# Kernel optimization log

Hardware: AMD Instinct MI355X
Metric: run time of the kernel (lower is better)

## Reference

```python
import jax, jax.numpy as jnp
import numpy as np

N_NODES = 100000


def gcn_conv(x, src, dst, W, b):
    # PyG GCNConv: add self-loops, symmetric deg^-1/2 normalization,
    # linear transform, scatter-add aggregation to target nodes, plus bias.
    n = x.shape[0]
    loops = jnp.arange(n, dtype=src.dtype)
    s = jnp.concatenate([src, loops])
    d = jnp.concatenate([dst, loops])
    deg = jax.ops.segment_sum(jnp.ones_like(s, dtype=x.dtype), d, num_segments=n)
    dinv = jnp.where(deg > 0, jax.lax.rsqrt(deg), 0.0)
    norm = dinv[s] * dinv[d]                       # [E+n]
    h = x @ W                                      # [n, out]
    msg = h[s] * norm[:, None]                     # gather + scale
    out = jax.ops.segment_sum(msg, d, num_segments=n)
    return out + b


def setup_inputs() -> dict:
    key = jax.random.key(0)
    k1, k2, k3, k4 = jax.random.split(key, 4)
    in_c, hid_c, out_c = 64, 64, 64
    n_edges = 1600000
    x = jax.random.normal(k1, (N_NODES, in_c), dtype=jnp.float32)
    edge_index = jax.random.randint(k2, (2, n_edges), 0, N_NODES, dtype=jnp.int64)
    W1 = jax.random.normal(k3, (in_c, hid_c), dtype=jnp.float32) * (1.0 / np.sqrt(in_c))
    b1 = jnp.zeros((hid_c,), dtype=jnp.float32)
    W2 = jax.random.normal(k4, (hid_c, out_c), dtype=jnp.float32) * (1.0 / np.sqrt(hid_c))
    b2 = jnp.zeros((out_c,), dtype=jnp.float32)
    return {"x": x, "edge_index": edge_index, "W1": W1, "b1": b1, "W2": W2, "b2": b2}


def reference(x, edge_index, W1, b1, W2, b2):
    src, dst = edge_index[0], edge_index[1]
    h = gcn_conv(x, src, dst, W1, b1)
    h = jax.nn.relu(h)
    out = gcn_conv(h, src, dst, W2, b2)
    return out
```

## Files before the change

kernel.cpp:

```cpp
#include <hip/hip_runtime.h>

#define NCH 64
#define NBLK 512
#define CB 512

typedef unsigned int uint;
typedef short short8 __attribute__((ext_vector_type(8)));
typedef float floatx4 __attribute__((ext_vector_type(4)));

__device__ inline uint bf16rne(float f) {
    uint u = __float_as_uint(f);
    return (u + 0x7fffu + ((u >> 16) & 1u)) >> 16;
}
__device__ inline uint pack2bf(float lo, float hi) {
    return bf16rne(lo) | (bf16rne(hi) << 16);
}
__device__ inline float unpLo(uint v) { return __uint_as_float(v << 16); }
__device__ inline float unpHi(uint v) { return __uint_as_float(v & 0xffff0000u); }

__device__ inline void pkadd(float2& acc, float lo, float hi) {
    float2 t = make_float2(lo, hi);
    asm("v_pk_add_f32 %0, %1, %2" : "=v"(acc) : "v"(acc), "v"(t));
}


__global__ void coarse_hist_kernel(const int* __restrict__ dst, int* __restrict__ cntCB,
                                   int ne, int epb) {
    __shared__ int h[CB];
    int t = threadIdx.x;
    for (int i = t; i < CB; i += blockDim.x) h[i] = 0;
    __syncthreads();
    int e0 = blockIdx.x * epb;
    int e1 = min(e0 + epb, ne);
    for (int e = e0 + t; e < e1; e += blockDim.x)
        atomicAdd(&h[dst[e] >> 8], 1);
    __syncthreads();
    for (int i = t; i < CB; i += blockDim.x) cntCB[i * NBLK + blockIdx.x] = h[i];
}

__global__ void binscan_kernel(int* __restrict__ cntCB, int* __restrict__ binTot) {
    __shared__ int s[NBLK];
    int bin = blockIdx.x;
    int t = threadIdx.x;
    int v = cntCB[bin * NBLK + t];
    s[t] = v;
    __syncthreads();
    for (int off = 1; off < NBLK; off <<= 1) {
        int add = (t >= off) ? s[t - off] : 0;
        __syncthreads();
        s[t] += add;
        __syncthreads();
    }
    cntCB[bin * NBLK + t] = s[t] - v;
    if (t == NBLK - 1) binTot[bin] = s[t];
}

__global__ void cbscan_kernel(const int* __restrict__ binTot, int* __restrict__ cb,
                              int* __restrict__ rowptr, int n, int ne) {
    __shared__ int s[CB];
    int t = threadIdx.x;
    int v = binTot[t];
    s[t] = v;
    __syncthreads();
    for (int off = 1; off < CB; off <<= 1) {
        int add = (t >= off) ? s[t - off] : 0;
        __syncthreads();
        s[t] += add;
        __syncthreads();
    }
    cb[t] = s[t] - v;
    if (t == CB - 1) { cb[CB] = ne; rowptr[n] = ne; }
}

__global__ void coarse_scatter_kernel(const int* __restrict__ src, const int* __restrict__ dst,
                                      const int* __restrict__ cntCB, const int* __restrict__ cb,
                                      uint* __restrict__ coarse, int ne, int epb) {
    __shared__ int cur[CB];
    int t = threadIdx.x;
    for (int i = t; i < CB; i += blockDim.x)
        cur[i] = cb[i] + cntCB[i * NBLK + blockIdx.x];
    __syncthreads();
    int e0 = blockIdx.x * epb;
    int e1 = min(e0 + epb, ne);
    for (int e = e0 + t; e < e1; e += blockDim.x) {
        int d = dst[e];
        int pos = atomicAdd(&cur[d >> 8], 1);
        coarse[pos] = ((uint)(d & 255) << 24) | (uint)src[e];
    }
}

__global__ void bucket_kernel(const uint* __restrict__ coarse, const int* __restrict__ cb,
                              int* __restrict__ rowptr, float* __restrict__ dinv,
                              int* __restrict__ csr, int n) {
    __shared__ int hist[256];
    __shared__ int excl[256];
    __shared__ int cursor[256];
    int k = blockIdx.x;
    int t = threadIdx.x;
    int base = cb[k];
    int end = cb[k + 1];
    hist[t] = 0;
    __syncthreads();
    for (int i = base + t; i < end; i += 256)
        atomicAdd(&hist[coarse[i] >> 24], 1);
    __syncthreads();
    int v = hist[t];
    excl[t] = v;
    __syncthreads();
    for (int off = 1; off < 256; off <<= 1) {
        int add = (t >= off) ? excl[t - off] : 0;
        __syncthreads();
        excl[t] += add;
        __syncthreads();
    }
    int ex = excl[t] - v;
    int node = (k << 8) + t;
    if (node < n) {
        rowptr[node] = base + ex;
        dinv[node] = rsqrtf(1.0f + (float)v);
    }
    cursor[t] = base + ex;
    __syncthreads();
    for (int i = base + t; i < end; i += 256) {
        uint e = coarse[i];
        int pos = atomicAdd(&cursor[e >> 24], 1);
        csr[pos] = (int)(e & 0x00FFFFFFu);
    }
}

__global__ void wfrag_kernel(const float* __restrict__ W1, const float* __restrict__ W2,
                             uint4* __restrict__ frag, uint* __restrict__ z1,
                             uint* __restrict__ z2, int n) {
    if (blockIdx.x == 4) {
        int t = threadIdx.x;
        if (t < 32) z1[(long long)n * 32 + t] = 0u;
        else if (t < 64) z2[(long long)n * 32 + (t - 32)] = 0u;
        return;
    }
    int tid = blockIdx.x * blockDim.x + threadIdx.x;
    int mat = tid >> 9;
    int rem = tid & 511;
    int nt = rem >> 7;
    int kb = (rem >> 6) & 1;
    int lane = rem & 63;
    const float* W = mat ? W2 : W1;
    int kbase = kb * 32 + (lane >> 4) * 8;
    int col = nt * 16 + (lane & 15);
    uint r[4];
#pragma unroll
    for (int j = 0; j < 4; ++j) {
        float lo = W[(kbase + 2 * j) * NCH + col];
        float hi = W[(kbase + 2 * j + 1) * NCH + col];
        r[j] = pack2bf(lo, hi);
    }
    frag[tid] = make_uint4(r[0], r[1], r[2], r[3]);
}

template<bool BF16A>
__global__ void gemm_mfma_kernel(const void* __restrict__ Xv, const uint4* __restrict__ wfrag,
                                 const float* __restrict__ dinv, uint* __restrict__ H, int n) {
    int lane = threadIdx.x & 63;
    int wave = blockIdx.x * (blockDim.x >> 6) + (threadIdx.x >> 6);
    int rb = wave * 16;
    if (rb >= n) return;

    short8 bfrag[4][2];
#pragma unroll
    for (int nt = 0; nt < 4; ++nt)
#pragma unroll
        for (int kb = 0; kb < 2; ++kb) {
            uint4 u = wfrag[(nt * 2 + kb) * 64 + lane];
            bfrag[nt][kb] = *(short8*)&u;
        }

    short8 afrag[2];
    if (BF16A) {
        const uint* hr = (const uint*)Xv + (long long)(rb + (lane & 15)) * 32 + (lane >> 4) * 8;
        uint4 a0 = *(const uint4*)(hr);
        uint4 a1 = *(const uint4*)(hr + 4);
        uint w[8] = {a0.x, a0.y, a0.z, a0.w, a1.x, a1.y, a1.z, a1.w};
        short8 f0, f1;
#pragma unroll
        for (int j = 0; j < 8; ++j) {
            f0[j] = (short)(w[j] & 0xffffu);
            f1[j] = (short)(w[j] >> 16);
        }
        afrag[0] = f0;
        afrag[1] = f1;
    } else {
        const float* xr = (const float*)Xv + (long long)(rb + (lane & 15)) * NCH + (lane >> 4) * 8;
#pragma unroll
        for (int kb = 0; kb < 2; ++kb) {
            float4 v0 = *(const float4*)(xr + kb * 32);
            float4 v1 = *(const float4*)(xr + kb * 32 + 4);
            short8 a;
            a[0] = (short)bf16rne(v0.x); a[1] = (short)bf16rne(v0.y);
            a[2] = (short)bf16rne(v0.z); a[3] = (short)bf16rne(v0.w);
            a[4] = (short)bf16rne(v1.x); a[5] = (short)bf16rne(v1.y);
            a[6] = (short)bf16rne(v1.z); a[7] = (short)bf16rne(v1.w);
            afrag[kb] = a;
        }
    }

    floatx4 acc[4];
#pragma unroll
    for (int nt = 0; nt < 4; ++nt) acc[nt] = (floatx4){0.f, 0.f, 0.f, 0.f};
#pragma unroll
    for (int nt = 0; nt < 4; ++nt)
#pragma unroll
        for (int kb = 0; kb < 2; ++kb)
            acc[nt] = __builtin_amdgcn_mfma_f32_16x16x32_bf16(afrag[kb], bfrag[nt][kb], acc[nt], 0, 0, 0);

    int r0 = rb + (lane >> 4) * 4;
#pragma unroll
    for (int reg = 0; reg < 4; ++reg) {
        float di = dinv[r0 + reg];
        long long roww = (long long)(r0 + reg) * 32;
#pragma unroll
        for (int nt = 0; nt < 2; ++nt) {
            int w = nt * 16 + (lane & 15);
            H[roww + w] = pack2bf(di * acc[nt][reg], di * acc[nt + 2][reg]);
        }
    }
}

template<bool BF16OUT>
__global__ void agg_kernel(const uint* __restrict__ hsB, const int* __restrict__ rowptr,
                           const int* __restrict__ csr, const float* __restrict__ dinv,
                           const float* __restrict__ b, void* __restrict__ outv, int n) {
    int wid = (blockIdx.x * blockDim.x + threadIdx.x) >> 6;
    if (wid >= n) return;
    wid = __builtin_amdgcn_readfirstlane(wid);
    int lane = threadIdx.x & 63;
    int o = lane >> 3;
    int u = lane & 7;
    int start = rowptr[wid];
    int end = rowptr[wid + 1];
    const uint4* __restrict__ base = (const uint4*)hsB + u;
    int ss = (o == 0) ? wid : n;
    uint4 v = base[(long long)ss * 8];
    float2 a0 = make_float2(unpLo(v.x), unpHi(v.x));
    float2 a1 = make_float2(unpLo(v.y), unpHi(v.y));
    float2 a2 = make_float2(unpLo(v.z), unpHi(v.z));
    float2 a3 = make_float2(unpLo(v.w), unpHi(v.w));
    for (int eb = start; eb < end; eb += 32) {
        int s0 = csr[eb + o];
        int s1 = csr[eb + 8 + o];
        int s2 = csr[eb + 16 + o];
        int s3 = csr[eb + 24 + o];
        s0 = (eb + o      < end) ? s0 : n;
        s1 = (eb + 8 + o  < end) ? s1 : n;
        s2 = (eb + 16 + o < end) ? s2 : n;
        s3 = (eb + 24 + o < end) ? s3 : n;
        uint4 g0 = base[(long long)s0 * 8];
        uint4 g1 = base[(long long)s1 * 8];
        uint4 g2 = base[(long long)s2 * 8];
        uint4 g3 = base[(long long)s3 * 8];
        pkadd(a0, unpLo(g0.x), unpHi(g0.x));
        pkadd(a1, unpLo(g0.y), unpHi(g0.y));
        pkadd(a2, unpLo(g0.z), unpHi(g0.z));
        pkadd(a3, unpLo(g0.w), unpHi(g0.w));
        pkadd(a0, unpLo(g1.x), unpHi(g1.x));
        pkadd(a1, unpLo(g1.y), unpHi(g1.y));
        pkadd(a2, unpLo(g1.z), unpHi(g1.z));
        pkadd(a3, unpLo(g1.w), unpHi(g1.w));
        pkadd(a0, unpLo(g2.x), unpHi(g2.x));
        pkadd(a1, unpLo(g2.y), unpHi(g2.y));
        pkadd(a2, unpLo(g2.z), unpHi(g2.z));
        pkadd(a3, unpLo(g2.w), unpHi(g2.w));
        pkadd(a0, unpLo(g3.x), unpHi(g3.x));
        pkadd(a1, unpLo(g3.y), unpHi(g3.y));
        pkadd(a2, unpLo(g3.z), unpHi(g3.z));
        pkadd(a3, unpLo(g3.w), unpHi(g3.w));
    }
#pragma unroll
    for (int m = 8; m <= 32; m <<= 1) {
        pkadd(a0, __shfl_xor(a0.x, m, 64), __shfl_xor(a0.y, m, 64));
        pkadd(a1, __shfl_xor(a1.x, m, 64), __shfl_xor(a1.y, m, 64));
        pkadd(a2, __shfl_xor(a2.x, m, 64), __shfl_xor(a2.y, m, 64));
        pkadd(a3, __shfl_xor(a3.x, m, 64), __shfl_xor(a3.y, m, 64));
    }
    if (o == 0) {
        float d = dinv[wid];
        float4 bl = *(const float4*)(b + 4 * u);
        float4 bh = *(const float4*)(b + 4 * u + 32);
        float r0l = d * a0.x + bl.x, r1l = d * a1.x + bl.y;
        float r2l = d * a2.x + bl.z, r3l = d * a3.x + bl.w;
        float r0h = d * a0.y + bh.x, r1h = d * a1.y + bh.y;
        float r2h = d * a2.y + bh.z, r3h = d * a3.y + bh.w;
        if (BF16OUT) {
            uint4 w;
            w.x = pack2bf(fmaxf(r0l, 0.f), fmaxf(r0h, 0.f));
            w.y = pack2bf(fmaxf(r1l, 0.f), fmaxf(r1h, 0.f));
            w.z = pack2bf(fmaxf(r2l, 0.f), fmaxf(r2h, 0.f));
            w.w = pack2bf(fmaxf(r3l, 0.f), fmaxf(r3h, 0.f));
            *((uint4*)outv + (long long)wid * 8 + u) = w;
        } else {
            float* out = (float*)outv + (long long)wid * NCH;
            *(float4*)(out + 4 * u) = make_float4(r0l, r1l, r2l, r3l);
            *(float4*)(out + 4 * u + 32) = make_float4(r0h, r1h, r2h, r3h);
        }
    }
}

extern "C" void kernel_launch(void* const* d_in, const int* in_sizes, int n_in,
                              void* d_out, int out_size, void* d_ws, size_t ws_size,
                              hipStream_t stream) {
    const float* x  = (const float*)d_in[0];
    const int*   ei = (const int*)d_in[1];
    const float* W1 = (const float*)d_in[2];
    const float* b1 = (const float*)d_in[3];
    const float* W2 = (const float*)d_in[4];
    const float* b2 = (const float*)d_in[5];
    const int n  = in_sizes[0] / NCH;
    const int ne = in_sizes[1] / 2;
    const int* src = ei;
    const int* dst = ei + ne;

    char* ws = (char*)d_ws;
    size_t off = 0;
    auto alloc = [&](size_t bytes) { void* p = ws + off; off += (bytes + 255) & ~(size_t)255; return p; };
    int*   cntCB   = (int*)alloc((size_t)CB * NBLK * 4);
    int*   binTot  = (int*)alloc((size_t)CB * 4);
    int*   cb      = (int*)alloc((size_t)(CB + 1) * 4);
    int*   rowptr  = (int*)alloc((size_t)(n + 1) * 4);
    float* dinv    = (float*)alloc((size_t)n * 4);
    int*   csr     = (int*)alloc((size_t)ne * 4 + 128);
    uint*  coarse  = (uint*)alloc((size_t)ne * 4);
    uint*  hsB     = (uint*)alloc((size_t)(n + 1) * 32 * 4);
    uint*  hsB2    = (uint*)alloc((size_t)(n + 1) * 32 * 4);
    uint4* wfrag   = (uint4*)alloc(1024 * 16);

    const int blk = 256;
    const int gAgg = (n * 64 + blk - 1) / blk;
    const int epb  = (ne + NBLK - 1) / NBLK;
    const int nBuck = (n + 255) / 256;
    const int nWaveG = (n + 15) / 16;
    const int gGemm = (nWaveG + 3) / 4;

    wfrag_kernel         <<<5, 256, 0, stream>>>(W1, W2, wfrag, hsB, hsB2, n);
    coarse_hist_kernel   <<<NBLK, blk, 0, stream>>>(dst, cntCB, ne, epb);
    binscan_kernel       <<<CB, NBLK, 0, stream>>>(cntCB, binTot);
    cbscan_kernel        <<<1, CB, 0, stream>>>(binTot, cb, rowptr, n, ne);
    coarse_scatter_kernel<<<NBLK, blk, 0, stream>>>(src, dst, cntCB, cb, coarse, ne, epb);
    bucket_kernel        <<<nBuck, 256, 0, stream>>>(coarse, cb, rowptr, dinv, csr, n);

    gemm_mfma_kernel<false><<<gGemm, blk, 0, stream>>>(x, wfrag, dinv, hsB, n);
    agg_kernel<true><<<gAgg, blk, 0, stream>>>(hsB, rowptr, csr, dinv, b1, hsB2, n);

    gemm_mfma_kernel<true><<<gGemm, blk, 0, stream>>>(hsB2, wfrag + 512, dinv, hsB, n);
    agg_kernel<false><<<gAgg, blk, 0, stream>>>(hsB, rowptr, csr, dinv, b2, d_out, n);
}
```

Baseline: 146.1 us.

## Add padded per-node 32-slot neighbor array so aggregation skips rowptr-dependent loads

The bucket kernel now also writes a fixed-width padded index array holding each node's first 32 source indices, with unused slots filled by the sentinel zero row. The aggregation kernel loads these indices with one aligned int4 per lane, independent of rowptr, so the first gathers can issue without waiting on rowptr and csr loads. Nodes with more than 32 neighbors fall back to the CSR loop for the rest. This adds 12.8 MB of index writes in the bucket pass and a larger workspace; with about 16 neighbors per node, most padded slots hold the sentinel.

```diff
diff --git a/kernel.cpp b/kernel.cpp
--- a/kernel.cpp
+++ b/kernel.cpp
@@ -91,10 +91,11 @@
 
 __global__ void bucket_kernel(const uint* __restrict__ coarse, const int* __restrict__ cb,
                               int* __restrict__ rowptr, float* __restrict__ dinv,
-                              int* __restrict__ csr, int n) {
+                              int* __restrict__ csr, int* __restrict__ csrPad, int n) {
     __shared__ int hist[256];
     __shared__ int excl[256];
     __shared__ int cursor[256];
+    __shared__ int startS[256];
     int k = blockIdx.x;
     int t = threadIdx.x;
     int base = cb[k];
@@ -118,13 +119,21 @@
     if (node < n) {
         rowptr[node] = base + ex;
         dinv[node] = rsqrtf(1.0f + (float)v);
+        for (int s = min(v, 32); s < 32; ++s)
+            csrPad[node * 32 + s] = n;
     }
     cursor[t] = base + ex;
+    startS[t] = base + ex;
     __syncthreads();
     for (int i = base + t; i < end; i += 256) {
         uint e = coarse[i];
-        int pos = atomicAdd(&cursor[e >> 24], 1);
-        csr[pos] = (int)(e & 0x00FFFFFFu);
+        int nd = e >> 24;
+        int sv = (int)(e & 0x00FFFFFFu);
+        int pos = atomicAdd(&cursor[nd], 1);
+        csr[pos] = sv;
+        int slot = pos - startS[nd];
+        if (slot < 32)
+            csrPad[(((k << 8) + nd)) * 32 + slot] = sv;
     }
 }
 
@@ -226,52 +235,76 @@
 
 template<bool BF16OUT>
 __global__ void agg_kernel(const uint* __restrict__ hsB, const int* __restrict__ rowptr,
-                           const int* __restrict__ csr, const float* __restrict__ dinv,
-                           const float* __restrict__ b, void* __restrict__ outv, int n) {
+                           const int* __restrict__ csr, const int* __restrict__ csrPad,
+                           const float* __restrict__ dinv, const float* __restrict__ b,
+                           void* __restrict__ outv, int n) {
     int wid = (blockIdx.x * blockDim.x + threadIdx.x) >> 6;
     if (wid >= n) return;
     wid = __builtin_amdgcn_readfirstlane(wid);
     int lane = threadIdx.x & 63;
     int o = lane >> 3;
     int u = lane & 7;
-    int start = rowptr[wid];
-    int end = rowptr[wid + 1];
     const uint4* __restrict__ base = (const uint4*)hsB + u;
+    int4 idx = ((const int4*)csrPad)[wid * 8 + o];
     int ss = (o == 0) ? wid : n;
     uint4 v = base[(long long)ss * 8];
     float2 a0 = make_float2(unpLo(v.x), unpHi(v.x));
     float2 a1 = make_float2(unpLo(v.y), unpHi(v.y));
     float2 a2 = make_float2(unpLo(v.z), unpHi(v.z));
     float2 a3 = make_float2(unpLo(v.w), unpHi(v.w));
-    for (int eb = start; eb < end; eb += 32) {
-        int s0 = csr[eb + o];
-        int s1 = csr[eb + 8 + o];
-        int s2 = csr[eb + 16 + o];
-        int s3 = csr[eb + 24 + o];
-        s0 = (eb + o      < end) ? s0 : n;
-        s1 = (eb + 8 + o  < end) ? s1 : n;
-        s2 = (eb + 16 + o < end) ? s2 : n;
-        s3 = (eb + 24 + o < end) ? s3 : n;
-        uint4 g0 = base[(long long)s0 * 8];
-        uint4 g1 = base[(long long)s1 * 8];
-        uint4 g2 = base[(long long)s2 * 8];
-        uint4 g3 = base[(long long)s3 * 8];
-        pkadd(a0, unpLo(g0.x), unpHi(g0.x));
-        pkadd(a1, unpLo(g0.y), unpHi(g0.y));
-        pkadd(a2, unpLo(g0.z), unpHi(g0.z));
-        pkadd(a3, unpLo(g0.w), unpHi(g0.w));
-        pkadd(a0, unpLo(g1.x), unpHi(g1.x));
-        pkadd(a1, unpLo(g1.y), unpHi(g1.y));
-        pkadd(a2, unpLo(g1.z), unpHi(g1.z));
-        pkadd(a3, unpLo(g1.w), unpHi(g1.w));
-        pkadd(a0, unpLo(g2.x), unpHi(g2.x));
-        pkadd(a1, unpLo(g2.y), unpHi(g2.y));
-        pkadd(a2, unpLo(g2.z), unpHi(g2.z));
-        pkadd(a3, unpLo(g2.w), unpHi(g2.w));
-        pkadd(a0, unpLo(g3.x), unpHi(g3.x));
-        pkadd(a1, unpLo(g3.y), unpHi(g3.y));
-        pkadd(a2, unpLo(g3.z), unpHi(g3.z));
-        pkadd(a3, unpLo(g3.w), unpHi(g3.w));
+    uint4 g0 = base[(long long)idx.x * 8];
+    uint4 g1 = base[(long long)idx.y * 8];
+    uint4 g2 = base[(long long)idx.z * 8];
+    uint4 g3 = base[(long long)idx.w * 8];
+    pkadd(a0, unpLo(g0.x), unpHi(g0.x));
+    pkadd(a1, unpLo(g0.y), unpHi(g0.y));
+    pkadd(a2, unpLo(g0.z), unpHi(g0.z));
+    pkadd(a3, unpLo(g0.w), unpHi(g0.w));
+    pkadd(a0, unpLo(g1.x), unpHi(g1.x));
+    pkadd(a1, unpLo(g1.y), unpHi(g1.y));
+    pkadd(a2, unpLo(g1.z), unpHi(g1.z));
+    pkadd(a3, unpLo(g1.w), unpHi(g1.w));
+    pkadd(a0, unpLo(g2.x), unpHi(g2.x));
+    pkadd(a1, unpLo(g2.y), unpHi(g2.y));
+    pkadd(a2, unpLo(g2.z), unpHi(g2.z));
+    pkadd(a3, unpLo(g2.w), unpHi(g2.w));
+    pkadd(a0, unpLo(g3.x), unpHi(g3.x));
+    pkadd(a1, unpLo(g3.y), unpHi(g3.y));
+    pkadd(a2, unpLo(g3.z), unpHi(g3.z));
+    pkadd(a3, unpLo(g3.w), unpHi(g3.w));
+    int start = rowptr[wid];
+    int end = rowptr[wid + 1];
+    if (end - start > 32) {
+        for (int eb = start + 32; eb < end; eb += 32) {
+            int s0 = csr[eb + o];
+            int s1 = csr[eb + 8 + o];
+            int s2 = csr[eb + 16 + o];
+            int s3 = csr[eb + 24 + o];
+            s0 = (eb + o      < end) ? s0 : n;
+            s1 = (eb + 8 + o  < end) ? s1 : n;
+            s2 = (eb + 16 + o < end) ? s2 : n;
+            s3 = (eb + 24 + o < end) ? s3 : n;
+            uint4 h0 = base[(long long)s0 * 8];
+            uint4 h1 = base[(long long)s1 * 8];
+            uint4 h2 = base[(long long)s2 * 8];
+            uint4 h3 = base[(long long)s3 * 8];
+            pkadd(a0, unpLo(h0.x), unpHi(h0.x));
+            pkadd(a1, unpLo(h0.y), unpHi(h0.y));
+            pkadd(a2, unpLo(h0.z), unpHi(h0.z));
+            pkadd(a3, unpLo(h0.w), unpHi(h0.w));
+            pkadd(a0, unpLo(h1.x), unpHi(h1.x));
+            pkadd(a1, unpLo(h1.y), unpHi(h1.y));
+            pkadd(a2, unpLo(h1.z), unpHi(h1.z));
+            pkadd(a3, unpLo(h1.w), unpHi(h1.w));
+            pkadd(a0, unpLo(h2.x), unpHi(h2.x));
+            pkadd(a1, unpLo(h2.y), unpHi(h2.y));
+            pkadd(a2, unpLo(h2.z), unpHi(h2.z));
+            pkadd(a3, unpLo(h2.w), unpHi(h2.w));
+            pkadd(a0, unpLo(h3.x), unpHi(h3.x));
+            pkadd(a1, unpLo(h3.y), unpHi(h3.y));
+            pkadd(a2, unpLo(h3.z), unpHi(h3.z));
+            pkadd(a3, unpLo(h3.w), unpHi(h3.w));
+        }
     }
 #pragma unroll
     for (int m = 8; m <= 32; m <<= 1) {
@@ -326,6 +359,7 @@
     int*   rowptr  = (int*)alloc((size_t)(n + 1) * 4);
     float* dinv    = (float*)alloc((size_t)n * 4);
     int*   csr     = (int*)alloc((size_t)ne * 4 + 128);
+    int*   csrPad  = (int*)alloc((size_t)n * 32 * 4);
     uint*  coarse  = (uint*)alloc((size_t)ne * 4);
     uint*  hsB     = (uint*)alloc((size_t)(n + 1) * 32 * 4);
     uint*  hsB2    = (uint*)alloc((size_t)(n + 1) * 32 * 4);
@@ -343,11 +377,11 @@
     binscan_kernel       <<<CB, NBLK, 0, stream>>>(cntCB, binTot);
     cbscan_kernel        <<<1, CB, 0, stream>>>(binTot, cb, rowptr, n, ne);
     coarse_scatter_kernel<<<NBLK, blk, 0, stream>>>(src, dst, cntCB, cb, coarse, ne, epb);
-    bucket_kernel        <<<nBuck, 256, 0, stream>>>(coarse, cb, rowptr, dinv, csr, n);
+    bucket_kernel        <<<nBuck, 256, 0, stream>>>(coarse, cb, rowptr, dinv, csr, csrPad, n);
 
     gemm_mfma_kernel<false><<<gGemm, blk, 0, stream>>>(x, wfrag, dinv, hsB, n);
-    agg_kernel<true><<<gAgg, blk, 0, stream>>>(hsB, rowptr, csr, dinv, b1, hsB2, n);
+    agg_kernel<true><<<gAgg, blk, 0, stream>>>(hsB, rowptr, csr, csrPad, dinv, b1, hsB2, n);
 
     gemm_mfma_kernel<true><<<gGemm, blk, 0, stream>>>(hsB2, wfrag + 512, dinv, hsB, n);
-    agg_kernel<false><<<gAgg, blk, 0, stream>>>(hsB, rowptr, csr, dinv, b2, d_out, n);
-}
+    agg_kernel<false><<<gAgg, blk, 0, stream>>>(hsB, rowptr, csr, csrPad, dinv, b2, d_out, n);
+}
```

Measured after the change: 150.1 us. 2.7% more time.
